# Kernel optimization log

Measured on AMD Instinct MI355X. Metric: run time of the kernel, lower is better.

The kernel has to match this reference:

```python
import jax, jax.numpy as jnp
import numpy as np

IN_C = 64
OUT_C = 64
NUM_RELS = 32
N_NODES = 20000
N_EDGES = 50000


def setup_inputs() -> dict:
    key = jax.random.key(0)
    k1, k2, k3, k4, k5, k6, k7 = jax.random.split(key, 7)
    x = jax.random.normal(k1, (N_NODES, IN_C), dtype=jnp.float32)
    edge_index = jax.random.randint(k2, (2, N_EDGES), 0, N_NODES, dtype=jnp.int64)
    edge_type = jax.random.randint(k3, (N_EDGES,), 0, NUM_RELS, dtype=jnp.int64)
    weight_fwd = jax.random.normal(k4, (NUM_RELS, IN_C * OUT_C), dtype=jnp.float32)
    weight_bwd = jax.random.normal(k5, (NUM_RELS, IN_C * OUT_C), dtype=jnp.float32)
    lin_w = jax.random.normal(k6, (OUT_C, IN_C), dtype=jnp.float32) * (1.0 / np.sqrt(IN_C))
    lin_b = jax.random.normal(k7, (OUT_C,), dtype=jnp.float32) * 0.01
    return {"x": x, "edge_index": edge_index, "edge_type": edge_type,
            "weight_fwd": weight_fwd, "weight_bwd": weight_bwd,
            "lin_w": lin_w, "lin_b": lin_b}


def type_gcn_conv(x, src, dst, edge_type, weight_table):
    # degrees[e] = (# edges sharing src[e]) + 1  (faithful to pairwise-compare count)
    n_nodes = x.shape[0]
    counts = jax.ops.segment_sum(jnp.ones(src.shape[0], jnp.float32), src,
                                 num_segments=n_nodes)
    degrees = counts[src] + 1.0                      # [E]
    w = weight_table[edge_type]                      # [E, in*out] gather
    w = w / (jnp.linalg.norm(w, axis=1, keepdims=True) + 0.01)
    w = w / degrees[:, None]
    w = w.reshape(-1, IN_C, OUT_C)                   # [E, in, out]
    msg = jnp.einsum('ei,eio->eo', x[src], w)        # per-edge small matmul
    return jax.ops.segment_sum(msg, dst, num_segments=n_nodes)  # scatter-add at dst


def reference(x, edge_index, edge_type, weight_fwd, weight_bwd, lin_w, lin_b):
    src, dst = edge_index[0], edge_index[1]
    fwd = type_gcn_conv(x, src, dst, edge_type, weight_fwd)
    # backward conv sees reversed edge_index: its src is original dst
    bwd = type_gcn_conv(x, dst, src, edge_type, weight_bwd)
    return x @ lin_w.T + lin_b + fwd + bwd
```

## Files before the change

### kernel.cpp

```cpp
#include <hip/hip_runtime.h>

#define NREL 32

typedef short short8 __attribute__((ext_vector_type(8)));
typedef float f32x4 __attribute__((ext_vector_type(4)));

__device__ inline unsigned short f2bf(float f) {
    union { float f; unsigned u; } u; u.f = f;
    unsigned r = u.u + 0x7FFF + ((u.u >> 16) & 1);
    return (unsigned short)(r >> 16);
}


__global__ __launch_bounds__(256) void setup_kernel(
        const float* __restrict__ x,
        const int* __restrict__ src, const int* __restrict__ dst,
        const int* __restrict__ et,
        const float* __restrict__ wf, const float* __restrict__ wb,
        const float* __restrict__ lw, const float* __restrict__ lb,
        float* __restrict__ cntf, float* __restrict__ cntb,
        int* __restrict__ fill, unsigned short* __restrict__ wtb,
        unsigned short* __restrict__ xbf, int2* __restrict__ einfo,
        float* __restrict__ out, int E, int N, int nCountB, int CAP) {
    __shared__ float smem[4 * 8 * 64 + 8];
    int tid = threadIdx.x;
    int b = blockIdx.x;

    if (b < nCountB) {
        int* lh = (int*)smem;
        int* lbase = lh + NREL;
        if (tid < 2 * NREL) lh[tid] = 0;
        __syncthreads();
        int e = b * 256 + tid;
        int s = 0, d = 0, r = 0, my = 0;
        bool valid = (e < E);
        if (valid) {
            s = src[e]; d = dst[e]; r = et[e];
            atomicAdd(&cntf[s], 1.0f);
            atomicAdd(&cntb[d], 1.0f);
            my = atomicAdd(&lh[r], 1);
        }
        __syncthreads();
        if (tid < NREL && lh[tid]) lbase[tid] = atomicAdd(&fill[tid], lh[tid]);
        __syncthreads();
        if (valid) einfo[r * CAP + lbase[r] + my] = make_int2(s, d);
        return;
    }
    b -= nCountB;
    if (b < 64) {
        int rel = b & 31, tab = b >> 5;
        const float* s_ = (tab ? wb : wf) + rel * 4096;
        unsigned short* d_ = wtb + (size_t)b * 4096;
        float* part = smem;
        float ssum = 0.f;
        #pragma unroll
        for (int k = 0; k < 16; k += 4) {
            float4 v = *(const float4*)(s_ + tid * 16 + k);
            ssum += v.x * v.x + v.y * v.y + v.z * v.z + v.w * v.w;
        }
        #pragma unroll
        for (int off = 32; off >= 1; off >>= 1) ssum += __shfl_down(ssum, off, 64);
        if ((tid & 63) == 0) part[tid >> 6] = ssum;
        __syncthreads();
        if (tid == 0) part[4] = 1.0f / (sqrtf(part[0] + part[1] + part[2] + part[3]) + 0.01f);
        __syncthreads();
        float sc = part[4];
        int i = tid >> 2, o0 = (tid & 3) * 16;
        #pragma unroll
        for (int q = 0; q < 4; ++q) {
            float4 v = *(const float4*)(s_ + i * 64 + o0 + q * 4);
            d_[(o0 + q * 4 + 0) * 64 + i] = f2bf(v.x * sc);
            d_[(o0 + q * 4 + 1) * 64 + i] = f2bf(v.y * sc);
            d_[(o0 + q * 4 + 2) * 64 + i] = f2bf(v.z * sc);
            d_[(o0 + q * 4 + 3) * 64 + i] = f2bf(v.w * sc);
        }
        return;
    }
    b -= 64;
    {
        int lane = tid & 63, w = tid >> 6;
        int nodeBase = b * 32 + w * 8;
        float4 wrow[16];
        const float4* lwrow = (const float4*)(lw + lane * 64);
        #pragma unroll
        for (int g = 0; g < 16; ++g) wrow[g] = lwrow[g];
        float bias = lb[lane];
        float* xs = smem + w * 8 * 64;
        #pragma unroll
        for (int t = 0; t < 8; ++t) {
            int n = nodeBase + t;
            if (n < N) {
                float v = x[(size_t)n * 64 + lane];
                xs[t * 64 + lane] = v;
                xbf[(size_t)n * 64 + lane] = f2bf(v);
            }
        }
        __syncthreads();
        for (int t = 0; t < 8; ++t) {
            int n = nodeBase + t;
            if (n >= N) break;
            float acc = bias;
            const float4* xr = (const float4*)(xs + t * 64);
            #pragma unroll
            for (int g = 0; g < 16; ++g) {
                float4 xv = xr[g];
                acc = fmaf(xv.x, wrow[g].x, acc);
                acc = fmaf(xv.y, wrow[g].y, acc);
                acc = fmaf(xv.z, wrow[g].z, acc);
                acc = fmaf(xv.w, wrow[g].w, acc);
            }
            out[(size_t)n * 64 + lane] = acc;
        }
    }
}

#define APITCH 72
__global__ __launch_bounds__(256) void conv_mfma(
        const unsigned short* __restrict__ xbf,
        const float* __restrict__ cntf, const float* __restrict__ cntb,
        const int* __restrict__ fill,
        const unsigned short* __restrict__ wtb,
        const int2* __restrict__ einfo,
        float* __restrict__ out, int CAP) {
    int tid = threadIdx.x;
    int lane = tid & 63;

    int fr = (lane < NREL) ? fill[lane] : 0;
    int ch = (fr + 63) >> 6;
    int s_scan = ch;
    #pragma unroll
    for (int off = 1; off < 32; off <<= 1) {
        int t = __shfl_up(s_scan, off, 64);
        if ((lane & 31) >= off) s_scan += t;
    }
    int chExcl = s_scan - ch;

    int c = blockIdx.x;
    unsigned long long mm = __ballot(lane < NREL && c >= chExcl && c < chExcl + ch);
    if (mm == 0) return;
    int rel = __ffsll(mm) - 1;
    int lc = c - __shfl(chExcl, rel, 64);
    int frr = __shfl(fr, rel, 64);
    int pos = rel * CAP + lc * 64;
    int valid = frr - lc * 64;
    if (valid > 64) valid = 64;

    __shared__ unsigned short Af[64 * APITCH];
    __shared__ unsigned short Ab[64 * APITCH];
    __shared__ unsigned short Bf[64 * APITCH];
    __shared__ unsigned short Bb[64 * APITCH];
    __shared__ int dstF[64], dstB[64];
    __shared__ float invF[64], invB[64];

    int j = tid >> 2, part = tid & 3;

    {
        size_t off = (size_t)rel * 4096 + j * 64 + part * 16;
        const uint4* sf = (const uint4*)(wtb + off);
        const uint4* sb = (const uint4*)(wtb + (size_t)NREL * 4096 + off);
        uint4 f0 = sf[0], f1 = sf[1], b0 = sb[0], b1 = sb[1];
        *(uint4*)(&Bf[j * APITCH + part * 16]) = f0;
        *(uint4*)(&Bf[j * APITCH + part * 16 + 8]) = f1;
        *(uint4*)(&Bb[j * APITCH + part * 16]) = b0;
        *(uint4*)(&Bb[j * APITCH + part * 16 + 8]) = b1;
    }

    if (j >= valid) {
        uint4 z = {0, 0, 0, 0};
        *(uint4*)(&Af[j * APITCH + part * 16]) = z;
        *(uint4*)(&Af[j * APITCH + part * 16 + 8]) = z;
        *(uint4*)(&Ab[j * APITCH + part * 16]) = z;
        *(uint4*)(&Ab[j * APITCH + part * 16 + 8]) = z;
        if (part == 0) { dstF[j] = -1; dstB[j] = -1; invF[j] = 0.f; invB[j] = 0.f; }
    } else {
        int2 v = einfo[pos + j];
        const uint4* xs = (const uint4*)(xbf + (size_t)v.x * 64);
        const uint4* xd = (const uint4*)(xbf + (size_t)v.y * 64);
        uint4 s0 = xs[part * 2], s1 = xs[part * 2 + 1];
        uint4 d0 = xd[part * 2], d1 = xd[part * 2 + 1];
        *(uint4*)(&Af[j * APITCH + part * 16]) = s0;
        *(uint4*)(&Af[j * APITCH + part * 16 + 8]) = s1;
        *(uint4*)(&Ab[j * APITCH + part * 16]) = d0;
        *(uint4*)(&Ab[j * APITCH + part * 16 + 8]) = d1;
        if (part == 0) {
            dstF[j] = v.y;  invF[j] = 1.0f / (cntf[v.x] + 1.0f);
            dstB[j] = v.x;  invB[j] = 1.0f / (cntb[v.y] + 1.0f);
        }
    }
    __syncthreads();

    int w = tid >> 6;
    int m = lane & 15, quad = lane >> 4;
    f32x4 zero4 = {0.f, 0.f, 0.f, 0.f};
    f32x4 accF[4] = {zero4, zero4, zero4, zero4};
    f32x4 accB[4] = {zero4, zero4, zero4, zero4};
    #pragma unroll
    for (int k0 = 0; k0 < 64; k0 += 32) {
        short8 aF = *(const short8*)(&Af[(w * 16 + m) * APITCH + k0 + quad * 8]);
        short8 aB = *(const short8*)(&Ab[(w * 16 + m) * APITCH + k0 + quad * 8]);
        #pragma unroll
        for (int n = 0; n < 4; ++n) {
            short8 bF = *(const short8*)(&Bf[(n * 16 + m) * APITCH + k0 + quad * 8]);
            short8 bB = *(const short8*)(&Bb[(n * 16 + m) * APITCH + k0 + quad * 8]);
            accF[n] = __builtin_amdgcn_mfma_f32_16x16x32_bf16(aF, bF, accF[n], 0, 0, 0);
            accB[n] = __builtin_amdgcn_mfma_f32_16x16x32_bf16(aB, bB, accB[n], 0, 0, 0);
        }
    }

    int row_base = w * 16 + quad * 4;
    #pragma unroll
    for (int r = 0; r < 4; ++r) {
        int row = row_base + r;
        int dF = dstF[row];
        if (dF >= 0) {
            float inv = invF[row];
            float* op = out + (size_t)dF * 64 + m;
            atomicAdd(op +  0, accF[0][r] * inv);
            atomicAdd(op + 16, accF[1][r] * inv);
            atomicAdd(op + 32, accF[2][r] * inv);
            atomicAdd(op + 48, accF[3][r] * inv);
        }
        int dB = dstB[row];
        if (dB >= 0) {
            float inv = invB[row];
            float* op = out + (size_t)dB * 64 + m;
            atomicAdd(op +  0, accB[0][r] * inv);
            atomicAdd(op + 16, accB[1][r] * inv);
            atomicAdd(op + 32, accB[2][r] * inv);
            atomicAdd(op + 48, accB[3][r] * inv);
        }
    }
}

extern "C" void kernel_launch(void* const* d_in, const int* in_sizes, int n_in,
                              void* d_out, int out_size, void* d_ws, size_t ws_size,
                              hipStream_t stream) {
    const float* x  = (const float*)d_in[0];
    const int*   ei = (const int*)  d_in[1];
    const int*   et = (const int*)  d_in[2];
    const float* wf = (const float*)d_in[3];
    const float* wb = (const float*)d_in[4];
    const float* lw = (const float*)d_in[5];
    const float* lb = (const float*)d_in[6];
    float* out = (float*)d_out;

    const int E = in_sizes[2];
    const int N = in_sizes[0] / 64;
    const int CAP = ((E + 63) >> 6) << 6;
    const int maxC = ((E + 63) >> 6) + NREL;

    char* p = (char*)d_ws;
    unsigned short* wtb = (unsigned short*)p;  p += (size_t)2 * NREL * 4096 * sizeof(unsigned short);
    unsigned short* xbf = (unsigned short*)p;  p += (size_t)N * 64 * sizeof(unsigned short);
    float* cntf = (float*)p;                   p += (size_t)N * sizeof(float);
    float* cntb = (float*)p;                   p += (size_t)N * sizeof(float);
    int*   fill = (int*)p;                     p += NREL * sizeof(int);
    int2*  einfo = (int2*)p;                   p += (size_t)NREL * CAP * sizeof(int2);

    const int* srcp = ei;
    const int* dstp = ei + E;

    hipMemsetAsync(cntf, 0, ((size_t)2 * N + NREL) * sizeof(float), stream);

    const int nCountB = (E + 255) / 256;
    const int nLinB   = (N + 31) / 32;
    setup_kernel<<<nCountB + 64 + nLinB, 256, 0, stream>>>(
        x, srcp, dstp, et, wf, wb, lw, lb, cntf, cntb, fill, wtb, xbf, einfo,
        out, E, N, nCountB, CAP);
    conv_mfma<<<maxC, 256, 0, stream>>>(xbf, cntf, cntb, fill, wtb, einfo, out, CAP);
}
```

Baseline: 113.2 us.

## Replace atomic scatter-add with per-edge message buffers and CSR gather reduction

Instead of float atomics into the output at destination nodes, the MFMA kernel now writes scaled per-edge messages to two E×64 buffers. Integer degree counts are prefix-scanned in a single-block offsets kernel, a CSR fill kernel records edge ids per node, and a reduce kernel gathers each node's messages and adds them to the output. This removes atomic contention and makes the sum order deterministic, at the cost of three extra launches, a serial single-block scan over all nodes, and about 25 MB of extra message traffic.

```diff
diff --git a/kernel.cpp b/kernel.cpp
--- a/kernel.cpp
+++ b/kernel.cpp
@@ -18,9 +18,9 @@
         const int* __restrict__ et,
         const float* __restrict__ wf, const float* __restrict__ wb,
         const float* __restrict__ lw, const float* __restrict__ lb,
-        float* __restrict__ cntf, float* __restrict__ cntb,
+        int* __restrict__ cntf, int* __restrict__ cntb,
         int* __restrict__ fill, unsigned short* __restrict__ wtb,
-        unsigned short* __restrict__ xbf, int2* __restrict__ einfo,
+        unsigned short* __restrict__ xbf, int4* __restrict__ einfo,
         float* __restrict__ out, int E, int N, int nCountB, int CAP) {
     __shared__ float smem[4 * 8 * 64 + 8];
     int tid = threadIdx.x;
@@ -36,14 +36,14 @@
         bool valid = (e < E);
         if (valid) {
             s = src[e]; d = dst[e]; r = et[e];
-            atomicAdd(&cntf[s], 1.0f);
-            atomicAdd(&cntb[d], 1.0f);
+            atomicAdd(&cntf[s], 1);
+            atomicAdd(&cntb[d], 1);
             my = atomicAdd(&lh[r], 1);
         }
         __syncthreads();
         if (tid < NREL && lh[tid]) lbase[tid] = atomicAdd(&fill[tid], lh[tid]);
         __syncthreads();
-        if (valid) einfo[r * CAP + lbase[r] + my] = make_int2(s, d);
+        if (valid) einfo[r * CAP + lbase[r] + my] = make_int4(s, d, e, 0);
         return;
     }
     b -= nCountB;
@@ -114,14 +114,62 @@
     }
 }
 
+__global__ __launch_bounds__(1024) void offsets_kernel(
+        const int* __restrict__ cntf, const int* __restrict__ cntb,
+        int* __restrict__ curS, int* __restrict__ curD,
+        float* __restrict__ invF, float* __restrict__ invB, int N) {
+    __shared__ int wsum[16];
+    __shared__ int wexcl[16];
+    int tid = threadIdx.x, lane = tid & 63, wv = tid >> 6;
+    int per = (N + 1023) >> 10;
+    for (int pass = 0; pass < 2; ++pass) {
+        const int* c = pass ? cntb : cntf;
+        int* cur = pass ? curD : curS;
+        float* ivd = pass ? invB : invF;
+        int base = tid * per;
+        int sum = 0;
+        for (int i = 0; i < per; ++i) { int n = base + i; if (n < N) sum += c[n]; }
+        int v = sum;
+        #pragma unroll
+        for (int off = 1; off < 64; off <<= 1) {
+            int t = __shfl_up(v, off, 64);
+            if (lane >= off) v += t;
+        }
+        if (lane == 63) wsum[wv] = v;
+        __syncthreads();
+        if (tid == 0) { int a = 0; for (int q = 0; q < 16; ++q) { wexcl[q] = a; a += wsum[q]; } }
+        __syncthreads();
+        int run = wexcl[wv] + (v - sum);
+        for (int i = 0; i < per; ++i) {
+            int n = base + i;
+            if (n < N) {
+                int cn = c[n];
+                cur[n] = run;
+                ivd[n] = 1.0f / (float)(cn + 1);
+                run += cn;
+            }
+        }
+        __syncthreads();
+    }
+}
+
+__global__ void csrfill_kernel(const int* __restrict__ src, const int* __restrict__ dst,
+                               int* __restrict__ curS, int* __restrict__ curD,
+                               int* __restrict__ csrS, int* __restrict__ csrD, int E) {
+    int e = blockIdx.x * 256 + threadIdx.x;
+    if (e >= E) return;
+    int pS = atomicAdd(&curS[src[e]], 1); csrS[pS] = e;
+    int pD = atomicAdd(&curD[dst[e]], 1); csrD[pD] = e;
+}
+
 #define APITCH 72
 __global__ __launch_bounds__(256) void conv_mfma(
         const unsigned short* __restrict__ xbf,
-        const float* __restrict__ cntf, const float* __restrict__ cntb,
+        const float* __restrict__ invF, const float* __restrict__ invB,
         const int* __restrict__ fill,
         const unsigned short* __restrict__ wtb,
-        const int2* __restrict__ einfo,
-        float* __restrict__ out, int CAP) {
+        const int4* __restrict__ einfo,
+        float* __restrict__ msgF, float* __restrict__ msgB, int CAP) {
     int tid = threadIdx.x;
     int lane = tid & 63;
 
@@ -149,8 +197,8 @@
     __shared__ unsigned short Ab[64 * APITCH];
     __shared__ unsigned short Bf[64 * APITCH];
     __shared__ unsigned short Bb[64 * APITCH];
-    __shared__ int dstF[64], dstB[64];
-    __shared__ float invF[64], invB[64];
+    __shared__ int eS[64];
+    __shared__ float ivF[64], ivB[64];
 
     int j = tid >> 2, part = tid & 3;
 
@@ -171,9 +219,9 @@
         *(uint4*)(&Af[j * APITCH + part * 16 + 8]) = z;
         *(uint4*)(&Ab[j * APITCH + part * 16]) = z;
         *(uint4*)(&Ab[j * APITCH + part * 16 + 8]) = z;
-        if (part == 0) { dstF[j] = -1; dstB[j] = -1; invF[j] = 0.f; invB[j] = 0.f; }
+        if (part == 0) { eS[j] = -1; ivF[j] = 0.f; ivB[j] = 0.f; }
     } else {
-        int2 v = einfo[pos + j];
+        int4 v = einfo[pos + j];
         const uint4* xs = (const uint4*)(xbf + (size_t)v.x * 64);
         const uint4* xd = (const uint4*)(xbf + (size_t)v.y * 64);
         uint4 s0 = xs[part * 2], s1 = xs[part * 2 + 1];
@@ -183,8 +231,9 @@
         *(uint4*)(&Ab[j * APITCH + part * 16]) = d0;
         *(uint4*)(&Ab[j * APITCH + part * 16 + 8]) = d1;
         if (part == 0) {
-            dstF[j] = v.y;  invF[j] = 1.0f / (cntf[v.x] + 1.0f);
-            dstB[j] = v.x;  invB[j] = 1.0f / (cntb[v.y] + 1.0f);
+            eS[j] = v.z;
+            ivF[j] = invF[v.x];
+            ivB[j] = invB[v.y];
         }
     }
     __syncthreads();
@@ -211,25 +260,44 @@
     #pragma unroll
     for (int r = 0; r < 4; ++r) {
         int row = row_base + r;
-        int dF = dstF[row];
-        if (dF >= 0) {
-            float inv = invF[row];
-            float* op = out + (size_t)dF * 64 + m;
-            atomicAdd(op +  0, accF[0][r] * inv);
-            atomicAdd(op + 16, accF[1][r] * inv);
-            atomicAdd(op + 32, accF[2][r] * inv);
-            atomicAdd(op + 48, accF[3][r] * inv);
-        }
-        int dB = dstB[row];
-        if (dB >= 0) {
-            float inv = invB[row];
-            float* op = out + (size_t)dB * 64 + m;
-            atomicAdd(op +  0, accB[0][r] * inv);
-            atomicAdd(op + 16, accB[1][r] * inv);
-            atomicAdd(op + 32, accB[2][r] * inv);
-            atomicAdd(op + 48, accB[3][r] * inv);
-        }
-    }
+        int e = eS[row];
+        if (e >= 0) {
+            float a = ivF[row], bsc = ivB[row];
+            float* pf = msgF + (size_t)e * 64 + m;
+            float* pb = msgB + (size_t)e * 64 + m;
+            pf[ 0] = accF[0][r] * a;
+            pf[16] = accF[1][r] * a;
+            pf[32] = accF[2][r] * a;
+            pf[48] = accF[3][r] * a;
+            pb[ 0] = accB[0][r] * bsc;
+            pb[16] = accB[1][r] * bsc;
+            pb[32] = accB[2][r] * bsc;
+            pb[48] = accB[3][r] * bsc;
+        }
+    }
+}
+
+__global__ __launch_bounds__(256) void reduce_kernel(
+        const int* __restrict__ cntf, const int* __restrict__ cntb,
+        const int* __restrict__ curS, const int* __restrict__ curD,
+        const int* __restrict__ csrS, const int* __restrict__ csrD,
+        const float* __restrict__ msgF, const float* __restrict__ msgB,
+        float* __restrict__ out, int N) {
+    int tid = threadIdx.x, lane = tid & 63, w = tid >> 6;
+    int n = blockIdx.x * 4 + w;
+    if (n >= N) return;
+    float acc = 0.f;
+    int eD = curD[n], cD = cntb[n];
+    for (int k = eD - cD; k < eD; ++k) {
+        int e = csrD[k];
+        acc += msgF[(size_t)e * 64 + lane];
+    }
+    int eS_ = curS[n], cS = cntf[n];
+    for (int k = eS_ - cS; k < eS_; ++k) {
+        int e = csrS[k];
+        acc += msgB[(size_t)e * 64 + lane];
+    }
+    out[(size_t)n * 64 + lane] += acc;
 }
 
 extern "C" void kernel_launch(void* const* d_in, const int* in_sizes, int n_in,
@@ -252,20 +320,33 @@
     char* p = (char*)d_ws;
     unsigned short* wtb = (unsigned short*)p;  p += (size_t)2 * NREL * 4096 * sizeof(unsigned short);
     unsigned short* xbf = (unsigned short*)p;  p += (size_t)N * 64 * sizeof(unsigned short);
-    float* cntf = (float*)p;                   p += (size_t)N * sizeof(float);
-    float* cntb = (float*)p;                   p += (size_t)N * sizeof(float);
-    int*   fill = (int*)p;                     p += NREL * sizeof(int);
-    int2*  einfo = (int2*)p;                   p += (size_t)NREL * CAP * sizeof(int2);
+    int*   cntf = (int*)p;                     p += (size_t)N * sizeof(int);
+    int*   cntb = (int*)p;                     p += (size_t)N * sizeof(int);
+    int*   fill = (int*)p;                     p += 32 * sizeof(int);
+    int*   curS = (int*)p;                     p += (size_t)N * sizeof(int);
+    int*   curD = (int*)p;                     p += (size_t)N * sizeof(int);
+    float* invF = (float*)p;                   p += (size_t)N * sizeof(float);
+    float* invB = (float*)p;                   p += (size_t)N * sizeof(float);
+    int*   csrS = (int*)p;                     p += (size_t)E * sizeof(int);
+    int*   csrD = (int*)p;                     p += (size_t)E * sizeof(int);
+    p = (char*)(((size_t)p + 15) & ~(size_t)15);
+    int4*  einfo = (int4*)p;                   p += (size_t)NREL * CAP * sizeof(int4);
+    float* msgF = (float*)p;                   p += (size_t)E * 64 * sizeof(float);
+    float* msgB = (float*)p;                   p += (size_t)E * 64 * sizeof(float);
 
     const int* srcp = ei;
     const int* dstp = ei + E;
 
-    hipMemsetAsync(cntf, 0, ((size_t)2 * N + NREL) * sizeof(float), stream);
+    hipMemsetAsync(cntf, 0, ((size_t)2 * N + NREL) * sizeof(int), stream);
 
     const int nCountB = (E + 255) / 256;
     const int nLinB   = (N + 31) / 32;
     setup_kernel<<<nCountB + 64 + nLinB, 256, 0, stream>>>(
         x, srcp, dstp, et, wf, wb, lw, lb, cntf, cntb, fill, wtb, xbf, einfo,
         out, E, N, nCountB, CAP);
-    conv_mfma<<<maxC, 256, 0, stream>>>(xbf, cntf, cntb, fill, wtb, einfo, out, CAP);
-}
+    offsets_kernel<<<1, 1024, 0, stream>>>(cntf, cntb, curS, curD, invF, invB, N);
+    csrfill_kernel<<<(E + 255) / 256, 256, 0, stream>>>(srcp, dstp, curS, curD, csrS, csrD, E);
+    conv_mfma<<<maxC, 256, 0, stream>>>(xbf, invF, invB, fill, wtb, einfo, msgF, msgB, CAP);
+    reduce_kernel<<<(N + 3) / 4, 256, 0, stream>>>(cntf, cntb, curS, curD, csrS, csrD,
+                                                   msgF, msgB, out, N);
+}
```

After: 193.1 us. 1.71x slower.
